# Kernel tuning notes

Hardware: AMD Instinct MI355X
Metric: run time of the kernel (lower is better)

Reference implementation:

```python
import jax, jax.numpy as jnp
import numpy as np

DIM = 1024
N_HEADS = 16
HEAD_DIM = DIM // N_HEADS


def setup_inputs() -> dict:
    key = jax.random.key(0)
    ks = jax.random.split(key, 9)
    s = 0.02
    return {
        "x": jax.random.normal(ks[0], (2, 2048, DIM), dtype=jnp.float32),
        "Wq": jax.random.normal(ks[1], (DIM, DIM), dtype=jnp.float32) * s,
        "bq": jax.random.normal(ks[2], (DIM,), dtype=jnp.float32) * s,
        "Wk": jax.random.normal(ks[3], (DIM, DIM), dtype=jnp.float32) * s,
        "bk": jax.random.normal(ks[4], (DIM,), dtype=jnp.float32) * s,
        "Wv": jax.random.normal(ks[5], (DIM, DIM), dtype=jnp.float32) * s,
        "bv": jax.random.normal(ks[6], (DIM,), dtype=jnp.float32) * s,
        "Wo": jax.random.normal(ks[7], (DIM, DIM), dtype=jnp.float32) * s,
        "bo": jax.random.normal(ks[8], (DIM,), dtype=jnp.float32) * s,
    }


def reference(x, Wq, bq, Wk, bk, Wv, bv, Wo, bo):
    B, T, C = x.shape
    # QKV projections, split heads -> [B, H, T, D]
    def split_heads(t):
        return t.reshape(B, T, N_HEADS, HEAD_DIM).transpose(0, 2, 1, 3)
    q = split_heads(x @ Wq + bq)
    k = split_heads(x @ Wk + bk)
    v = split_heads(x @ Wv + bv)
    scale = 1.0 / jnp.sqrt(jnp.float32(HEAD_DIM))
    scores = jnp.einsum("bhqd,bhkd->bhqk", q, k) * scale  # [B,H,T,T]
    causal = jnp.tril(jnp.ones((T, T), dtype=bool))  # True = keep
    scores = jnp.where(causal, scores, jnp.float32(-jnp.inf))
    weights = jax.nn.softmax(scores, axis=-1)
    ctx = jnp.einsum("bhqk,bhkd->bhqd", weights, v)
    ctx = ctx.transpose(0, 2, 1, 3).reshape(B, T, C)
    return ctx @ Wo + bo
```

## Files before the change

### kernel.cpp

```cpp
#include <hip/hip_runtime.h>
#include <hip/hip_bf16.h>
#include <stdint.h>

#define DIM    1024
#define SEQ    2048
#define NB     2
#define NH     16
#define HD     64
#define NROWS  (NB*SEQ)

typedef unsigned short u16;
typedef __attribute__((ext_vector_type(8))) short bf16x8;
typedef __attribute__((ext_vector_type(4))) float f32x4;
typedef __attribute__((ext_vector_type(4))) unsigned short u16x4;

#define NEG_INF (-__builtin_inff())

__device__ __forceinline__ u16 f2bf(float f) {
    union { float f; uint32_t u; } x; x.f = f;
    uint32_t r = x.u + 0x7FFFu + ((x.u >> 16) & 1u);
    return (u16)(r >> 16);
}

__device__ __forceinline__ void gload_lds16(const void* g, void* l) {
    __builtin_amdgcn_global_load_lds(
        (const __attribute__((address_space(1))) void*)g,
        (__attribute__((address_space(3))) void*)l, 16, 0, 0);
}

__global__ __launch_bounds__(256)
void cvt_x(const float* __restrict__ in, u16* __restrict__ out)
{
    size_t i = (size_t)blockIdx.x * 256 + threadIdx.x;
    float4 f = *(const float4*)&in[i * 4];
    u16x4 o = { f2bf(f.x), f2bf(f.y), f2bf(f.z), f2bf(f.w) };
    *(u16x4*)&out[i * 4] = o;
}

__global__ __launch_bounds__(256)
void cvt_w(const float* __restrict__ Wq, const float* __restrict__ Wk,
           const float* __restrict__ Wv, const float* __restrict__ Wo,
           u16* __restrict__ Wqt, u16* __restrict__ Wkt,
           u16* __restrict__ Wvt, u16* __restrict__ Wot)
{
    __shared__ u16 Ws[64][68];
    const int z = blockIdx.z;
    const float* W = z == 0 ? Wq : z == 1 ? Wk : z == 2 ? Wv : Wo;
    u16* Wt        = z == 0 ? Wqt : z == 1 ? Wkt : z == 2 ? Wvt : Wot;
    const int k0 = blockIdx.x * 64;
    const int n0 = blockIdx.y * 64;
    const int tid = threadIdx.x;

    #pragma unroll
    for (int it = 0; it < 4; ++it) {
        int idx = tid + it * 256;
        int r = idx >> 4, cq = idx & 15;
        float4 f = *(const float4*)&W[(size_t)(k0 + r) * DIM + n0 + cq * 4];
        u16x4 o = { f2bf(f.x), f2bf(f.y), f2bf(f.z), f2bf(f.w) };
        *(u16x4*)&Ws[r][cq * 4] = o;
    }
    __syncthreads();
    #pragma unroll
    for (int it = 0; it < 4; ++it) {
        int idx = tid + it * 256;
        int rr = idx >> 4, cq = idx & 15;
        u16x4 o = { Ws[cq*4+0][rr], Ws[cq*4+1][rr], Ws[cq*4+2][rr], Ws[cq*4+3][rr] };
        *(u16x4*)&Wt[(size_t)(n0 + rr) * DIM + k0 + cq * 4] = o;
    }
}

template<int MODE>
__global__ __launch_bounds__(256)
void gemm_mfma(const u16* __restrict__ A,
               const u16* __restrict__ Wt0, const u16* __restrict__ Wt1,
               const u16* __restrict__ Wt2,
               const float* __restrict__ b0, const float* __restrict__ b1,
               const float* __restrict__ b2,
               void* __restrict__ o0, void* __restrict__ o1, void* __restrict__ o2)
{
    __shared__ __align__(16) uint8_t lds[32768];
    uint8_t* Asb = lds;
    uint8_t* Bsb = lds + 16384;

    const int tid  = threadIdx.x;
    const int wid  = tid >> 6, lane = tid & 63;
    const int lr   = lane & 15, lg = lane >> 4;
    const int wr   = wid >> 1, wc = wid & 1;

    const int r0 = blockIdx.x * 128;
    const int c0 = blockIdx.y * 128;

    const u16* Wt; const float* bias; u16* obf = nullptr; float* ofp = nullptr;
    int cw; float qscale = 1.0f;
    if (MODE == 0) {
        int sel = c0 >> 10;
        cw  = c0 & 1023;
        Wt   = sel == 0 ? Wt0 : sel == 1 ? Wt1 : Wt2;
        bias = sel == 0 ? b0  : sel == 1 ? b1  : b2;
        obf  = (u16*)(sel == 0 ? o0 : sel == 1 ? o1 : o2);
        if (sel == 0) qscale = 0.125f;
    } else {
        cw = c0; Wt = Wt0; bias = b0; ofp = (float*)o0;
    }

    f32x4 acc[4][4] = {};

    for (int k0 = 0; k0 < DIM; k0 += 64) {
        __syncthreads();
        #pragma unroll
        for (int seg = 0; seg < 4; ++seg) {
            int o   = seg * 4096 + tid * 16;
            int row = o >> 7;
            int sch = ((o >> 4) & 7) ^ (row & 7);
            gload_lds16((const uint8_t*)A  + ((size_t)(r0 + row) << 11) + (k0 << 1) + (sch << 4),
                        Asb + seg * 4096 + (wid << 10) + (lane << 4));
            gload_lds16((const uint8_t*)Wt + ((size_t)(cw + row) << 11) + (k0 << 1) + (sch << 4),
                        Bsb + seg * 4096 + (wid << 10) + (lane << 4));
        }
        __syncthreads();

        __builtin_amdgcn_s_setprio(1);
        #pragma unroll
        for (int kk = 0; kk < 2; ++kk) {
            bf16x8 a[4], b[4];
            #pragma unroll
            for (int i = 0; i < 4; ++i) {
                int ar = wr * 64 + i * 16 + lr;
                a[i] = *(const bf16x8*)(Asb + ar * 128 + ((((kk << 2) | lg) ^ (ar & 7)) << 4));
                int br = wc * 64 + i * 16 + lr;
                b[i] = *(const bf16x8*)(Bsb + br * 128 + ((((kk << 2) | lg) ^ (br & 7)) << 4));
            }
            #pragma unroll
            for (int i = 0; i < 4; ++i)
                #pragma unroll
                for (int j = 0; j < 4; ++j)
                    acc[i][j] = __builtin_amdgcn_mfma_f32_16x16x32_bf16(a[i], b[j], acc[i][j], 0, 0, 0);
        }
        __builtin_amdgcn_s_setprio(0);
    }

    #pragma unroll
    for (int j = 0; j < 4; ++j) {
        int colw = wc * 64 + j * 16 + lr;
        float bv = bias[cw + colw];
        #pragma unroll
        for (int i = 0; i < 4; ++i) {
            #pragma unroll
            for (int r = 0; r < 4; ++r) {
                float val = (acc[i][j][r] + bv) * qscale;
                int row = r0 + wr * 64 + i * 16 + lg * 4 + r;
                if (MODE == 0) {
                    int col = cw + colw;
                    int h = col >> 6, d = col & 63;
                    int bb = row >> 11, t = row & (SEQ - 1);
                    obf[((((size_t)bb * NH + h) * SEQ + t) << 6) + d] = f2bf(val);
                } else {
                    ofp[((size_t)row << 10) + c0 + colw] = val;
                }
            }
        }
    }
}

__global__ __launch_bounds__(256)
void attn_mfma(const u16* __restrict__ q, const u16* __restrict__ k,
               const u16* __restrict__ v, u16* __restrict__ ctx)
{
    __shared__ __align__(16) uint8_t lds[24576];
    uint8_t* Qs = lds;
    uint8_t* Ks = lds + 8192;
    uint8_t* Vt = lds + 16384;

    const int tid = threadIdx.x;
    const int wid = tid >> 6, lane = tid & 63;
    const int lr  = lane & 15, lg = lane >> 4;

    const int n  = blockIdx.x;
    const int j4 = n >> 8;
    const int c  = n & 255;
    const int ch = c >> 5;
    const int bh = c & 31;
    const int qt = (j4 == 0) ? ch : (j4 == 1) ? (15 - ch)
                 : (j4 == 2) ? (16 + ch) : (31 - ch);

    const size_t hb = (size_t)bh * SEQ * HD;
    const int q0 = qt * 64;

    #pragma unroll
    for (int seg = 0; seg < 2; ++seg) {
        int o = seg * 4096 + tid * 16;
        int row = o >> 7;
        int sch = ((o >> 4) & 7) ^ (row & 7);
        gload_lds16((const uint8_t*)(q + hb) + (size_t)(q0 + row) * 128 + (sch << 4),
                    Qs + seg * 4096 + (wid << 10) + (lane << 4));
    }

    const int vp = tid >> 3;
    const int vg = tid & 7;
    const int vj  = vp >> 3;
    const int vlg = (vp >> 1) & 3;
    const int vrr = (vp & 1) * 2;
    const int vslot = (vj & 1) * 32 + vlg * 8 + ((vj >> 1) << 2) + vrr;

    f32x4 acc[4] = {};
    float m_own = NEG_INF;
    float l_own = 0.f;
    bf16x8 aQ0, aQ1;

    for (int kt = 0; kt <= qt; ++kt) {
        __syncthreads();
        #pragma unroll
        for (int seg = 0; seg < 2; ++seg) {
            int o = seg * 4096 + tid * 16;
            int row = o >> 7;
            int sch = ((o >> 4) & 7) ^ (row & 7);
            gload_lds16((const uint8_t*)(k + hb) + (size_t)(kt * 64 + row) * 128 + (sch << 4),
                        Ks + seg * 4096 + (wid << 10) + (lane << 4));
        }
        {
            const u16* vsrc = v + hb + ((size_t)(kt * 64 + 2 * vp) << 6) + vg * 8;
            bf16x8 v0 = *(const bf16x8*)vsrc;
            bf16x8 v1 = *(const bf16x8*)(vsrc + 64);
            #pragma unroll
            for (int i = 0; i < 8; ++i) {
                int d = vg * 8 + i;
                int swzd = (d ^ (d >> 3)) & 7;
                uint32_t w = (uint32_t)(u16)v0[i] | ((uint32_t)(u16)v1[i] << 16);
                *(uint32_t*)(Vt + d * 128 + ((((vslot >> 3) ^ swzd) << 4))
                             + ((vslot & 7) << 1)) = w;
            }
        }
        __syncthreads();

        if (kt == 0) {
            int qr = wid * 16 + lr;
            aQ0 = *(const bf16x8*)(Qs + qr * 128 + ((lg       ^ (qr & 7)) << 4));
            aQ1 = *(const bf16x8*)(Qs + qr * 128 + (((4 | lg) ^ (qr & 7)) << 4));
        }

        f32x4 s[4];
        __builtin_amdgcn_s_setprio(1);
        #pragma unroll
        for (int j = 0; j < 4; ++j) {
            int krow = j * 16 + lr;
            bf16x8 b0 = *(const bf16x8*)(Ks + krow * 128 + ((lg       ^ (krow & 7)) << 4));
            bf16x8 b1 = *(const bf16x8*)(Ks + krow * 128 + (((4 | lg) ^ (krow & 7)) << 4));
            f32x4 z = {0.f, 0.f, 0.f, 0.f};
            z    = __builtin_amdgcn_mfma_f32_16x16x32_bf16(b0, aQ0, z, 0, 0, 0);
            s[j] = __builtin_amdgcn_mfma_f32_16x16x32_bf16(b1, aQ1, z, 0, 0, 0);
        }
        __builtin_amdgcn_s_setprio(0);

        if (kt == qt) {
            #pragma unroll
            for (int j = 0; j < 4; ++j)
                #pragma unroll
                for (int r = 0; r < 4; ++r)
                    if (j * 16 + lg * 4 + r > wid * 16 + lr) s[j][r] = NEG_INF;
        }

        float rm = NEG_INF;
        #pragma unroll
        for (int j = 0; j < 4; ++j) {
            float a = fmaxf(fmaxf(s[j][0], s[j][1]), fmaxf(s[j][2], s[j][3]));
            rm = fmaxf(rm, a);
        }
        rm = fmaxf(rm, __shfl_xor(rm, 16));
        rm = fmaxf(rm, __shfl_xor(rm, 32));
        float mnew = fmaxf(m_own, rm);
        float aown = __expf(m_own - mnew);
        m_own = mnew;

        float rs = 0.f;
        #pragma unroll
        for (int j = 0; j < 4; ++j)
            #pragma unroll
            for (int r = 0; r < 4; ++r) {
                float p = __expf(s[j][r] - mnew);
                s[j][r] = p;
                rs += p;
            }
        rs += __shfl_xor(rs, 16);
        rs += __shfl_xor(rs, 32);
        l_own = l_own * aown + rs;

        float ar[4];
        #pragma unroll
        for (int r = 0; r < 4; ++r) ar[r] = __shfl(aown, lg * 4 + r);
        #pragma unroll
        for (int ni = 0; ni < 4; ++ni)
            #pragma unroll
            for (int r = 0; r < 4; ++r)
                acc[ni][r] *= ar[r];

        bf16x8 pa0, pa1;
        #pragma unroll
        for (int i = 0; i < 4; ++i) {
            pa0[i]     = (short)f2bf(s[0][i]);
            pa0[4 + i] = (short)f2bf(s[2][i]);
            pa1[i]     = (short)f2bf(s[1][i]);
            pa1[4 + i] = (short)f2bf(s[3][i]);
        }

        __builtin_amdgcn_s_setprio(1);
        #pragma unroll
        for (int ni = 0; ni < 4; ++ni) {
            int vrow = ni * 16 + lr;
            int swzd = (vrow ^ (vrow >> 3)) & 7;
            bf16x8 vb0 = *(const bf16x8*)(Vt + vrow * 128 + ((lg       ^ swzd) << 4));
            bf16x8 vb1 = *(const bf16x8*)(Vt + vrow * 128 + (((4 | lg) ^ swzd) << 4));
            acc[ni] = __builtin_amdgcn_mfma_f32_16x16x32_bf16(pa0, vb0, acc[ni], 0, 0, 0);
            acc[ni] = __builtin_amdgcn_mfma_f32_16x16x32_bf16(pa1, vb1, acc[ni], 0, 0, 0);
        }
        __builtin_amdgcn_s_setprio(0);
    }

    float rinv = 1.f / l_own;
    float rl[4];
    #pragma unroll
    for (int r = 0; r < 4; ++r) rl[r] = __shfl(rinv, lg * 4 + r);

    const int b = bh >> 4, h = bh & 15;
    #pragma unroll
    for (int r = 0; r < 4; ++r) {
        int t = q0 + wid * 16 + lg * 4 + r;
        size_t base = (((size_t)b * SEQ + t) << 10) + (h << 6);
        #pragma unroll
        for (int ni = 0; ni < 4; ++ni)
            ctx[base + ni * 16 + lr] = f2bf(acc[ni][r] * rl[r]);
    }
}

extern "C" void kernel_launch(void* const* d_in, const int* in_sizes, int n_in,
                              void* d_out, int out_size, void* d_ws, size_t ws_size,
                              hipStream_t stream)
{
    (void)in_sizes; (void)n_in; (void)out_size; (void)ws_size;
    const float* x  = (const float*)d_in[0];
    const float* Wq = (const float*)d_in[1];
    const float* bq = (const float*)d_in[2];
    const float* Wk = (const float*)d_in[3];
    const float* bk = (const float*)d_in[4];
    const float* Wv = (const float*)d_in[5];
    const float* bv = (const float*)d_in[6];
    const float* Wo = (const float*)d_in[7];
    const float* bo = (const float*)d_in[8];

    u16* ws = (u16*)d_ws;
    const size_t M1 = (size_t)1024 * 1024;
    const size_t M4 = (size_t)NROWS * DIM;
    u16* xb  = ws;
    u16* wqt = ws + M4;
    u16* wkt = wqt + M1;
    u16* wvt = wkt + M1;
    u16* wot = wvt + M1;
    u16* qb  = wot + M1;
    u16* kb  = qb + M4;
    u16* vb  = kb + M4;
    u16* cb  = vb + M4;

    cvt_x<<<dim3(4096), dim3(256), 0, stream>>>(x, xb);
    cvt_w<<<dim3(16, 16, 4), dim3(256), 0, stream>>>(Wq, Wk, Wv, Wo, wqt, wkt, wvt, wot);
    gemm_mfma<0><<<dim3(32, 24), dim3(256), 0, stream>>>(
        xb, wqt, wkt, wvt, bq, bk, bv, qb, kb, vb);
    attn_mfma<<<dim3(1024), dim3(256), 0, stream>>>(qb, kb, vb, cb);
    gemm_mfma<1><<<dim3(32, 8), dim3(256), 0, stream>>>(
        cb, wot, nullptr, nullptr, bo, nullptr, nullptr, d_out, nullptr, nullptr);
}
```

Baseline: 190.8 us.

## Use exp2 softmax with lazy rescale, prefetch V, and packed bf16 converts

Folds log2(e) into the Q scale so the softmax can use exp2f instead of __expf. It skips rescaling the accumulator when the row max grows by no more than 8 (lazy rescaling). It also prefetches the next V tile into registers one iteration early to hide global-load latency. The manual bf16 rounding is replaced by the v_cvt_pk_bf16_f32 instruction. Lazy rescaling lets values exceed 1 before the bf16 conversion, which may cost a little precision; prefetching adds register pressure.

```diff
diff --git a/kernel.cpp b/kernel.cpp
--- a/kernel.cpp
+++ b/kernel.cpp
@@ -20,6 +20,12 @@
     union { float f; uint32_t u; } x; x.f = f;
     uint32_t r = x.u + 0x7FFFu + ((x.u >> 16) & 1u);
     return (u16)(r >> 16);
+}
+
+__device__ __forceinline__ uint32_t cvtpk(float a, float b) {
+    uint32_t r;
+    asm volatile("v_cvt_pk_bf16_f32 %0, %1, %2" : "=v"(r) : "v"(a), "v"(b));
+    return r;
 }
 
 __device__ __forceinline__ void gload_lds16(const void* g, void* l) {
@@ -98,7 +104,7 @@
         Wt   = sel == 0 ? Wt0 : sel == 1 ? Wt1 : Wt2;
         bias = sel == 0 ? b0  : sel == 1 ? b1  : b2;
         obf  = (u16*)(sel == 0 ? o0 : sel == 1 ? o1 : o2);
-        if (sel == 0) qscale = 0.125f;
+        if (sel == 0) qscale = 0.125f * 1.44269504088896f;
     } else {
         cw = c0; Wt = Wt0; bias = b0; ofp = (float*)o0;
     }
@@ -202,6 +208,11 @@
     const int vrr = (vp & 1) * 2;
     const int vslot = (vj & 1) * 32 + vlg * 8 + ((vj >> 1) << 2) + vrr;
 
+    const u16* vbase = v + hb + ((size_t)(2 * vp) << 6) + vg * 8;
+
+    bf16x8 vpre0 = *(const bf16x8*)(vbase);
+    bf16x8 vpre1 = *(const bf16x8*)(vbase + 64);
+
     f32x4 acc[4] = {};
     float m_own = NEG_INF;
     float l_own = 0.f;
@@ -218,19 +229,22 @@
                         Ks + seg * 4096 + (wid << 10) + (lane << 4));
         }
         {
-            const u16* vsrc = v + hb + ((size_t)(kt * 64 + 2 * vp) << 6) + vg * 8;
-            bf16x8 v0 = *(const bf16x8*)vsrc;
-            bf16x8 v1 = *(const bf16x8*)(vsrc + 64);
             #pragma unroll
             for (int i = 0; i < 8; ++i) {
                 int d = vg * 8 + i;
                 int swzd = (d ^ (d >> 3)) & 7;
-                uint32_t w = (uint32_t)(u16)v0[i] | ((uint32_t)(u16)v1[i] << 16);
+                uint32_t w = (uint32_t)(u16)vpre0[i] | ((uint32_t)(u16)vpre1[i] << 16);
                 *(uint32_t*)(Vt + d * 128 + ((((vslot >> 3) ^ swzd) << 4))
                              + ((vslot & 7) << 1)) = w;
             }
         }
         __syncthreads();
+
+        if (kt < qt) {
+            const u16* vsrc = vbase + ((size_t)(kt + 1) << 12);
+            vpre0 = *(const bf16x8*)(vsrc);
+            vpre1 = *(const bf16x8*)(vsrc + 64);
+        }
 
         if (kt == 0) {
             int qr = wid * 16 + lr;
@@ -267,40 +281,40 @@
         }
         rm = fmaxf(rm, __shfl_xor(rm, 16));
         rm = fmaxf(rm, __shfl_xor(rm, 32));
-        float mnew = fmaxf(m_own, rm);
-        float aown = __expf(m_own - mnew);
-        m_own = mnew;
+
+        if (!__all(rm <= m_own + 8.f)) {
+            float mnew = fmaxf(m_own, rm);
+            float aown = exp2f(m_own - mnew);
+            m_own = mnew;
+            l_own *= aown;
+            float ar[4];
+            #pragma unroll
+            for (int r = 0; r < 4; ++r) ar[r] = __shfl(aown, lg * 4 + r);
+            #pragma unroll
+            for (int ni = 0; ni < 4; ++ni)
+                #pragma unroll
+                for (int r = 0; r < 4; ++r)
+                    acc[ni][r] *= ar[r];
+        }
 
         float rs = 0.f;
         #pragma unroll
         for (int j = 0; j < 4; ++j)
             #pragma unroll
             for (int r = 0; r < 4; ++r) {
-                float p = __expf(s[j][r] - mnew);
+                float p = exp2f(s[j][r] - m_own);
                 s[j][r] = p;
                 rs += p;
             }
         rs += __shfl_xor(rs, 16);
         rs += __shfl_xor(rs, 32);
-        l_own = l_own * aown + rs;
-
-        float ar[4];
-        #pragma unroll
-        for (int r = 0; r < 4; ++r) ar[r] = __shfl(aown, lg * 4 + r);
-        #pragma unroll
-        for (int ni = 0; ni < 4; ++ni)
-            #pragma unroll
-            for (int r = 0; r < 4; ++r)
-                acc[ni][r] *= ar[r];
-
-        bf16x8 pa0, pa1;
-        #pragma unroll
-        for (int i = 0; i < 4; ++i) {
-            pa0[i]     = (short)f2bf(s[0][i]);
-            pa0[4 + i] = (short)f2bf(s[2][i]);
-            pa1[i]     = (short)f2bf(s[1][i]);
-            pa1[4 + i] = (short)f2bf(s[3][i]);
-        }
+        l_own += rs;
+
+        union { uint32_t u[4]; bf16x8 h; } P0, P1;
+        P0.u[0] = cvtpk(s[0][0], s[0][1]); P0.u[1] = cvtpk(s[0][2], s[0][3]);
+        P0.u[2] = cvtpk(s[2][0], s[2][1]); P0.u[3] = cvtpk(s[2][2], s[2][3]);
+        P1.u[0] = cvtpk(s[1][0], s[1][1]); P1.u[1] = cvtpk(s[1][2], s[1][3]);
+        P1.u[2] = cvtpk(s[3][0], s[3][1]); P1.u[3] = cvtpk(s[3][2], s[3][3]);
 
         __builtin_amdgcn_s_setprio(1);
         #pragma unroll
@@ -309,8 +323,8 @@
             int swzd = (vrow ^ (vrow >> 3)) & 7;
             bf16x8 vb0 = *(const bf16x8*)(Vt + vrow * 128 + ((lg       ^ swzd) << 4));
             bf16x8 vb1 = *(const bf16x8*)(Vt + vrow * 128 + (((4 | lg) ^ swzd) << 4));
-            acc[ni] = __builtin_amdgcn_mfma_f32_16x16x32_bf16(pa0, vb0, acc[ni], 0, 0, 0);
-            acc[ni] = __builtin_amdgcn_mfma_f32_16x16x32_bf16(pa1, vb1, acc[ni], 0, 0, 0);
+            acc[ni] = __builtin_amdgcn_mfma_f32_16x16x32_bf16(P0.h, vb0, acc[ni], 0, 0, 0);
+            acc[ni] = __builtin_amdgcn_mfma_f32_16x16x32_bf16(P1.h, vb1, acc[ni], 0, 0, 0);
         }
         __builtin_amdgcn_s_setprio(0);
     }
```

After: 195.1 us. 2.3% more time.
